# Kernel tuning notes

Measured on AMD Instinct MI355X. Metric: run time of the kernel, lower is better.

Reference implementation:

```python
import jax, jax.numpy as jnp
import numpy as np
import math

B, S, D, H = 2, 2048, 1024, 16
HD = D // H  # head dim = 64


def _rope_tables():
    # RoFormer sinusoidal position embedding: one frequency per (even, odd) pair
    pos = jnp.arange(S, dtype=jnp.float32)[:, None]                # [S, 1]
    inv_freq = 1.0 / (10000.0 ** (jnp.arange(0, HD, 2, dtype=jnp.float32) / HD))  # [HD/2]
    ang = pos * inv_freq[None, :]                                   # [S, HD/2]
    sin = jnp.sin(ang)[None, None]                                  # [1,1,S,HD/2]
    cos = jnp.cos(ang)[None, None]
    return sin, cos


def setup_inputs() -> dict:
    key = jax.random.key(0)
    k0, k1, k2, k3 = jax.random.split(key, 4)
    scale = 1.0 / math.sqrt(D)
    sin, cos = _rope_tables()
    return {
        "hidden_states": jax.random.normal(k0, (B, S, D), dtype=jnp.float32),
        "Wq": jax.random.normal(k1, (D, D), dtype=jnp.float32) * scale,
        "Wk": jax.random.normal(k2, (D, D), dtype=jnp.float32) * scale,
        "Wv": jax.random.normal(k3, (D, D), dtype=jnp.float32) * scale,
        "sin": sin,
        "cos": cos,
    }


def _split_heads(x):
    # [B,S,D] -> [B,H,S,HD]
    b, s, _ = x.shape
    return x.reshape(b, s, H, HD).transpose(0, 2, 1, 3)


def _apply_rotary(x, sin, cos):
    # x: [B,H,S,HD]; sin/cos broadcast as [1,1,S,HD/2]
    x1 = x[..., 0::2]
    x2 = x[..., 1::2]
    out = jnp.stack([x1 * cos - x2 * sin, x2 * cos + x1 * sin], axis=-1)
    return out.reshape(x.shape)


def reference(hidden_states, Wq, Wk, Wv, sin, cos):
    q = _apply_rotary(_split_heads(hidden_states @ Wq), sin, cos)  # [B,H,S,HD]
    k = _apply_rotary(_split_heads(hidden_states @ Wk), sin, cos)
    v = _apply_rotary(_split_heads(hidden_states @ Wv), sin, cos)  # note: RoPE on V too, per source
    scores = jnp.einsum("bhqd,bhkd->bhqk", q, k) / math.sqrt(HD)   # [B,H,S,S]
    probs = jax.nn.softmax(scores, axis=-1)
    ctx = jnp.einsum("bhqk,bhkd->bhqd", probs, v)                   # [B,H,S,HD]
    return ctx.transpose(0, 2, 1, 3).reshape(hidden_states.shape[0], S, D)
```

## Files before the change

### kernel.cpp

```cpp
#include <hip/hip_runtime.h>

typedef unsigned short u16;
typedef unsigned short u16x8 __attribute__((ext_vector_type(8)));
typedef unsigned short u16x4 __attribute__((ext_vector_type(4)));
typedef short s16x4 __attribute__((ext_vector_type(4)));
typedef __bf16 bf16x8_t __attribute__((ext_vector_type(8)));
typedef float floatx4 __attribute__((ext_vector_type(4)));

#define BATCH 2
#define S_LEN 2048
#define D_DIM 1024
#define NH    16
#define HD    64

__device__ __forceinline__ u16 f2b(float f) {
  union { float f; unsigned int i; } c; c.f = f;
  const unsigned int i = c.i;
  return (u16)((i + 0x7FFFu + ((i >> 16) & 1u)) >> 16);
}
__device__ __forceinline__ unsigned int fbits(float f) {
  union { float f; unsigned int i; } c; c.f = f; return c.i;
}
__device__ __forceinline__ bf16x8_t asbf(u16x8 v) {
  union { u16x8 u; bf16x8_t b; } c; c.u = v; return c.b;
}
__device__ __forceinline__ s16x4 as4(uint2 v) {
  union { uint2 u; s16x4 s; } c; c.u = v; return c.s;
}
__device__ __forceinline__ s16x4 as4u(u16x4 v) {
  union { u16x4 u; s16x4 s; } c; c.u = v; return c.s;
}
__device__ __forceinline__ void load_lds16(const u16* g, u16* l) {
  __builtin_amdgcn_global_load_lds(
      (const __attribute__((address_space(1))) void*)g,
      (__attribute__((address_space(3))) void*)l, 16, 0, 0);
}

__device__ __attribute__((aligned(256))) u16 g_xb[(size_t)BATCH * S_LEN * D_DIM];
__device__ __attribute__((aligned(256))) u16 g_wt[3u * D_DIM * D_DIM];
__device__ __attribute__((aligned(256))) u16 g_qkv[3u * BATCH * S_LEN * D_DIM];

__global__ __launch_bounds__(256) void prep(const float* __restrict__ X,
                                            const float* __restrict__ Wq,
                                            const float* __restrict__ Wk,
                                            const float* __restrict__ Wv) {
  const int tid = threadIdx.x;
  const int z = blockIdx.y;
  if (z == 3) {
#pragma unroll
    for (int c = 0; c < 8; ++c) {
      const size_t i = (((size_t)c * 256 + blockIdx.x) * 256 + tid) * 8;
      floatx4 a = *(const floatx4*)(X + i);
      floatx4 b = *(const floatx4*)(X + i + 4);
      u16x8 o;
#pragma unroll
      for (int j = 0; j < 4; ++j) { o[j] = f2b(a[j]); o[4 + j] = f2b(b[j]); }
      *(u16x8*)(g_xb + i) = o;
    }
    return;
  }
  __shared__ u16 t[64][65];
  const float* W = (z == 0) ? Wq : (z == 1) ? Wk : Wv;
  u16* Wt = g_wt + (size_t)z * D_DIM * D_DIM;
  const int k0 = (blockIdx.x & 15) * 64;
  const int n0 = (blockIdx.x >> 4) * 64;
  const int rr = tid >> 4;
  const int cc = (tid & 15) * 4;
#pragma unroll
  for (int i = 0; i < 4; ++i) {
    const int r = rr + i * 16;
    floatx4 v = *(const floatx4*)(W + (size_t)(k0 + r) * D_DIM + n0 + cc);
    t[r][cc] = f2b(v[0]); t[r][cc + 1] = f2b(v[1]);
    t[r][cc + 2] = f2b(v[2]); t[r][cc + 3] = f2b(v[3]);
  }
  __syncthreads();
#pragma unroll
  for (int i = 0; i < 4; ++i) {
    const int r = rr + i * 16;
    u16x4 v;
    v[0] = t[cc][r]; v[1] = t[cc + 1][r]; v[2] = t[cc + 2][r]; v[3] = t[cc + 3][r];
    *(u16x4*)(Wt + (size_t)(n0 + r) * D_DIM + k0 + cc) = v;
  }
}

__global__ __launch_bounds__(256) void qkv_gemm(const float* __restrict__ sin_t,
                                                const float* __restrict__ cos_t) {
  __shared__ __attribute__((aligned(16))) u16 lds_a[128 * 32];
  __shared__ __attribute__((aligned(16))) u16 lds_b[128 * 32];
  const int tid = threadIdx.x;
  const int wv = tid >> 6;
  const int lane = tid & 63;
  const int lrow = lane & 15;
  const int quad = lane >> 4;
  const int wr = wv >> 1, wc = wv & 1;
  const int m0 = blockIdx.x * 128;
  const int n0 = blockIdx.y * 128;
  const int z = blockIdx.z;
  const bool vmode = (z == 2);
  const u16* Wz = g_wt + (size_t)z * (D_DIM * D_DIM);

  floatx4 acc[4][4] = {};

  const u16* gA = g_xb + (size_t)(m0 + wv * 32 + (lane >> 2)) * D_DIM + (lane & 3) * 8;
  const u16* gB = Wz   + (size_t)(n0 + wv * 32 + (lane >> 2)) * D_DIM + (lane & 3) * 8;
  u16* sA = &lds_a[(wv * 32) * 32];
  u16* sB = &lds_b[(wv * 32) * 32];

  const u16* Aarr = vmode ? lds_a : lds_b;
  const u16* Barr = vmode ? lds_b : lds_a;

  for (int k0 = 0; k0 < D_DIM; k0 += 32) {
    __syncthreads();
    load_lds16(gA + k0, sA);
    load_lds16(gA + (size_t)16 * D_DIM + k0, sA + 512);
    load_lds16(gB + k0, sB);
    load_lds16(gB + (size_t)16 * D_DIM + k0, sB + 512);
    __syncthreads();
    u16x8 af[4], bfr[4];
#pragma unroll
    for (int mi = 0; mi < 4; ++mi)
      af[mi] = *(const u16x8*)&Aarr[(wr * 64 + mi * 16 + lrow) * 32 + quad * 8];
#pragma unroll
    for (int ni = 0; ni < 4; ++ni)
      bfr[ni] = *(const u16x8*)&Barr[(wc * 64 + ni * 16 + lrow) * 32 + quad * 8];
#pragma unroll
    for (int mi = 0; mi < 4; ++mi)
#pragma unroll
      for (int ni = 0; ni < 4; ++ni)
        acc[mi][ni] = __builtin_amdgcn_mfma_f32_16x16x32_bf16(
            asbf(af[mi]), asbf(bfr[ni]), acc[mi][ni], 0, 0, 0);
  }

  if (!vmode) {
    const float qsc = (z == 0) ? 0.18033688011112042f : 1.0f;
    u16* outz = g_qkv + (size_t)z * (BATCH * S_LEN * D_DIM);
#pragma unroll
    for (int mi = 0; mi < 4; ++mi) {
      const int nf0 = n0 + wr * 64 + mi * 16 + quad * 4;
      const int h = nf0 >> 6, hd0 = nf0 & 63, i00 = hd0 >> 1;
#pragma unroll
      for (int ni = 0; ni < 4; ++ni) {
        const int sg = m0 + wc * 64 + ni * 16 + lrow;
        const int b = sg >> 11, srow = sg & 2047;
        const float c0 = cos_t[(size_t)srow * 32 + i00];
        const float s0 = sin_t[(size_t)srow * 32 + i00];
        const float c1 = cos_t[(size_t)srow * 32 + i00 + 1];
        const float s1 = sin_t[(size_t)srow * 32 + i00 + 1];
        const float v0 = acc[mi][ni][0], v1 = acc[mi][ni][1];
        const float v2 = acc[mi][ni][2], v3 = acc[mi][ni][3];
        u16x4 ov;
        ov[0] = f2b((v0 * c0 - v1 * s0) * qsc);
        ov[1] = f2b((v1 * c0 + v0 * s0) * qsc);
        ov[2] = f2b((v2 * c1 - v3 * s1) * qsc);
        ov[3] = f2b((v3 * c1 + v2 * s1) * qsc);
        *(u16x4*)(outz + ((size_t)(b * NH + h) * S_LEN + srow) * HD + hd0) = ov;
      }
    }
  } else {
    u16* outv = g_qkv + (size_t)2 * (BATCH * S_LEN * D_DIM);
#pragma unroll
    for (int mi = 0; mi < 4; ++mi) {
      const int s0g = m0 + wr * 64 + mi * 16 + quad * 4;
      const int b = s0g >> 11, sl = s0g & 2047;
#pragma unroll
      for (int ni = 0; ni < 4; ++ni) {
        const int nf = n0 + wc * 64 + ni * 16 + lrow;
        const int h = nf >> 6, hd = nf & 63, i0 = hd >> 1;
        const float sgn = (hd & 1) ? 1.f : -1.f;
        u16x4 ov;
#pragma unroll
        for (int r = 0; r < 4; ++r) {
          const int s = sl + r;
          const float c  = cos_t[(size_t)s * 32 + i0];
          const float sn = sin_t[(size_t)s * 32 + i0];
          const float v  = acc[mi][ni][r];
          const float vp = __shfl_xor(v, 1);
          ov[r] = f2b(v * c + sgn * sn * vp);
        }
        *(u16x4*)(outv + ((size_t)(b * NH + h) * HD + hd) * S_LEN + sl) = ov;
      }
    }
  }
}

__global__ __launch_bounds__(256) void flash_attn(float* __restrict__ out) {
  __shared__ __attribute__((aligned(16))) u16 lds_k[2][64 * 72];
  __shared__ __attribute__((aligned(16))) u16 lds_v[2][64 * 72];
  const int bh = blockIdx.x;
  const int qt = blockIdx.y;
  const int b = bh >> 4, h = bh & 15;
  const int tid = threadIdx.x, wv = tid >> 6, lane = tid & 63;
  const int lrow = lane & 15, quad = lane >> 4;
  const u16* Qb  = g_qkv + (size_t)bh * (S_LEN * HD);
  const u16* Kb  = g_qkv + (size_t)(BATCH * NH + bh) * (S_LEN * HD);
  const u16* VTb = g_qkv + (size_t)(2 * BATCH * NH + bh) * (S_LEN * HD);
  const int q0 = qt * 64 + wv * 16;

  u16x8 qf[2];
#pragma unroll
  for (int ks = 0; ks < 2; ++ks)
    qf[ks] = *(const u16x8*)(Qb + (size_t)(q0 + lrow) * HD + ks * 32 + quad * 8);

  floatx4 oacc[4] = {};
  float l_part = 0.f;

  const int sr = tid >> 3;
  const int sc = (tid & 7) * 8;

  u16x8 kreg[2], vreg[2];
#pragma unroll
  for (int i = 0; i < 2; ++i) {
    const int r = sr + i * 32;
    kreg[i] = *(const u16x8*)(Kb + (size_t)r * HD + sc);
    vreg[i] = *(const u16x8*)(VTb + (size_t)r * S_LEN + sc);
  }

  for (int t = 0; t < S_LEN / 64; ++t) {
    const int buf = t & 1;
#pragma unroll
    for (int i = 0; i < 2; ++i) {
      const int r = sr + i * 32;
      *(u16x8*)&lds_k[buf][r * 72 + sc] = kreg[i];
      *(u16x8*)&lds_v[buf][r * 72 + sc] = vreg[i];
    }
    __syncthreads();
    if (t + 1 < S_LEN / 64) {
      const int kv0n = (t + 1) * 64;
#pragma unroll
      for (int i = 0; i < 2; ++i) {
        const int r = sr + i * 32;
        kreg[i] = *(const u16x8*)(Kb + (size_t)(kv0n + r) * HD + sc);
        vreg[i] = *(const u16x8*)(VTb + (size_t)r * S_LEN + kv0n + sc);
      }
    }

    floatx4 sacc[4] = {};
    __builtin_amdgcn_s_setprio(1);
#pragma unroll
    for (int nb = 0; nb < 4; ++nb)
#pragma unroll
      for (int ks = 0; ks < 2; ++ks) {
        u16x8 kf = *(const u16x8*)&lds_k[buf][(nb * 16 + lrow) * 72 + ks * 32 + quad * 8];
        sacc[nb] = __builtin_amdgcn_mfma_f32_16x16x32_bf16(
            asbf(kf), asbf(qf[ks]), sacc[nb], 0, 0, 0);
      }
    __builtin_amdgcn_s_setprio(0);

    uint2 pk[4];
#pragma unroll
    for (int nb = 0; nb < 4; ++nb) {
      const float p0 = __builtin_amdgcn_exp2f(sacc[nb][0]);
      const float p1 = __builtin_amdgcn_exp2f(sacc[nb][1]);
      const float p2 = __builtin_amdgcn_exp2f(sacc[nb][2]);
      const float p3 = __builtin_amdgcn_exp2f(sacc[nb][3]);
      l_part += (p0 + p1) + (p2 + p3);
      pk[nb].x = __byte_perm(fbits(p0), fbits(p1), 0x7632);
      pk[nb].y = __byte_perm(fbits(p2), fbits(p3), 0x7632);
    }

    __builtin_amdgcn_s_setprio(1);
#pragma unroll
    for (int nb = 0; nb < 4; ++nb) {
      const s16x4 pa = as4(pk[nb]);
#pragma unroll
      for (int hb = 0; hb < 4; ++hb) {
        u16x4 vf = *(const u16x4*)&lds_v[buf][(hb * 16 + lrow) * 72 + nb * 16 + quad * 4];
        oacc[hb] = __builtin_amdgcn_mfma_f32_16x16x16bf16_1k(
            pa, as4u(vf), oacc[hb], 0, 0, 0);
      }
    }
    __builtin_amdgcn_s_setprio(0);
  }

  float l = l_part;
  l += __shfl_xor(l, 16);
  l += __shfl_xor(l, 32);
  float linv[4];
#pragma unroll
  for (int r = 0; r < 4; ++r)
    linv[r] = 1.f / __shfl(l, quad * 4 + r);

#pragma unroll
  for (int hb = 0; hb < 4; ++hb) {
    const int hd = hb * 16 + lrow;
#pragma unroll
    for (int r = 0; r < 4; ++r) {
      const int q = q0 + quad * 4 + r;
      out[((size_t)(b * S_LEN) + q) * D_DIM + h * HD + hd] = oacc[hb][r] * linv[r];
    }
  }
}

extern "C" void kernel_launch(void* const* d_in, const int* in_sizes, int n_in,
                              void* d_out, int out_size, void* d_ws, size_t ws_size,
                              hipStream_t stream) {
  const float* X = (const float*)d_in[0];
  const float* sin_t = (const float*)d_in[4];
  const float* cos_t = (const float*)d_in[5];

  prep<<<dim3(256, 4), 256, 0, stream>>>(X, (const float*)d_in[1],
                                         (const float*)d_in[2],
                                         (const float*)d_in[3]);

  qkv_gemm<<<dim3(32, 8, 3), 256, 0, stream>>>(sin_t, cos_t);

  flash_attn<<<dim3(32, 32), 256, 0, stream>>>((float*)d_out);
}
```

Baseline: 193.2 us.

## Split KV across waves with register-direct fragment loads and LDS reduction

The attention kernel now gives each wave a quarter of every 64-key tile for all 64 queries, instead of one 16-query slice over all keys. K and V fragments are read straight from global memory into registers, double-buffered across tiles, so the per-tile LDS staging and barriers go away. The QKV GEMM epilogue writes V in a 4-interleaved layout so each lane's V fragment is one contiguous 8-byte load. Partial outputs and row sums are combined across waves at the end through LDS in four serialized phases. This raises register pressure (a 4x4 output accumulator per wave) and adds a final cross-wave reduction, in exchange for removing the LDS round trip and synchronisation inside the main loop.

```diff
diff --git a/kernel.cpp b/kernel.cpp
--- a/kernel.cpp
+++ b/kernel.cpp
@@ -177,15 +177,16 @@
           const float vp = __shfl_xor(v, 1);
           ov[r] = f2b(v * c + sgn * sn * vp);
         }
-        *(u16x4*)(outv + ((size_t)(b * NH + h) * HD + hd) * S_LEN + sl) = ov;
+        *(u16x4*)(outv + (size_t)(b * NH + h) * (S_LEN * HD) +
+                  ((size_t)(sl >> 2) * HD + hd) * 4) = ov;
       }
     }
   }
 }
 
 __global__ __launch_bounds__(256) void flash_attn(float* __restrict__ out) {
-  __shared__ __attribute__((aligned(16))) u16 lds_k[2][64 * 72];
-  __shared__ __attribute__((aligned(16))) u16 lds_v[2][64 * 72];
+  __shared__ float red[64 * 65];
+  __shared__ float lred[4 * 64];
   const int bh = blockIdx.x;
   const int qt = blockIdx.y;
   const int b = bh >> 4, h = bh & 15;
@@ -194,100 +195,111 @@
   const u16* Qb  = g_qkv + (size_t)bh * (S_LEN * HD);
   const u16* Kb  = g_qkv + (size_t)(BATCH * NH + bh) * (S_LEN * HD);
   const u16* VTb = g_qkv + (size_t)(2 * BATCH * NH + bh) * (S_LEN * HD);
-  const int q0 = qt * 64 + wv * 16;
-
-  u16x8 qf[2];
-#pragma unroll
-  for (int ks = 0; ks < 2; ++ks)
-    qf[ks] = *(const u16x8*)(Qb + (size_t)(q0 + lrow) * HD + ks * 32 + quad * 8);
-
-  floatx4 oacc[4] = {};
-  float l_part = 0.f;
-
-  const int sr = tid >> 3;
-  const int sc = (tid & 7) * 8;
-
-  u16x8 kreg[2], vreg[2];
-#pragma unroll
-  for (int i = 0; i < 2; ++i) {
-    const int r = sr + i * 32;
-    kreg[i] = *(const u16x8*)(Kb + (size_t)r * HD + sc);
-    vreg[i] = *(const u16x8*)(VTb + (size_t)r * S_LEN + sc);
-  }
-
-  for (int t = 0; t < S_LEN / 64; ++t) {
-    const int buf = t & 1;
-#pragma unroll
-    for (int i = 0; i < 2; ++i) {
-      const int r = sr + i * 32;
-      *(u16x8*)&lds_k[buf][r * 72 + sc] = kreg[i];
-      *(u16x8*)&lds_v[buf][r * 72 + sc] = vreg[i];
-    }
-    __syncthreads();
-    if (t + 1 < S_LEN / 64) {
-      const int kv0n = (t + 1) * 64;
-#pragma unroll
-      for (int i = 0; i < 2; ++i) {
-        const int r = sr + i * 32;
-        kreg[i] = *(const u16x8*)(Kb + (size_t)(kv0n + r) * HD + sc);
-        vreg[i] = *(const u16x8*)(VTb + (size_t)r * S_LEN + kv0n + sc);
-      }
-    }
-
-    floatx4 sacc[4] = {};
+  const int qbase = qt * 64;
+
+  u16x8 qf[4][2];
+#pragma unroll
+  for (int nb = 0; nb < 4; ++nb)
+#pragma unroll
+    for (int ks = 0; ks < 2; ++ks)
+      qf[nb][ks] = *(const u16x8*)(Qb + (size_t)(qbase + nb * 16 + lrow) * HD +
+                                   ks * 32 + quad * 8);
+
+  floatx4 oacc[4][4] = {};
+  float lacc[4] = {};
+
+  const u16* Kw = Kb + (size_t)(wv * 16 + lrow) * HD + quad * 8;
+  const u16* Vw = VTb + ((size_t)(wv * 4 + quad) * HD + lrow) * 4;
+
+  auto loadK = [&](u16x8* kr, int t) {
+    const u16* p = Kw + (size_t)t * 64 * HD;
+    kr[0] = *(const u16x8*)(p);
+    kr[1] = *(const u16x8*)(p + 32);
+  };
+  auto loadV = [&](u16x4* vr, int t) {
+    const u16* p = Vw + (size_t)t * 16 * HD * 4;
+#pragma unroll
+    for (int hb = 0; hb < 4; ++hb)
+      vr[hb] = *(const u16x4*)(p + hb * 16 * 4);
+  };
+  auto tile = [&](const u16x8* kr, const u16x4* vr) {
+    floatx4 sacc[4];
     __builtin_amdgcn_s_setprio(1);
 #pragma unroll
-    for (int nb = 0; nb < 4; ++nb)
-#pragma unroll
-      for (int ks = 0; ks < 2; ++ks) {
-        u16x8 kf = *(const u16x8*)&lds_k[buf][(nb * 16 + lrow) * 72 + ks * 32 + quad * 8];
-        sacc[nb] = __builtin_amdgcn_mfma_f32_16x16x32_bf16(
-            asbf(kf), asbf(qf[ks]), sacc[nb], 0, 0, 0);
-      }
+    for (int nb = 0; nb < 4; ++nb) {
+      floatx4 s0 = {};
+      s0 = __builtin_amdgcn_mfma_f32_16x16x32_bf16(asbf(kr[0]), asbf(qf[nb][0]), s0, 0, 0, 0);
+      sacc[nb] = __builtin_amdgcn_mfma_f32_16x16x32_bf16(asbf(kr[1]), asbf(qf[nb][1]), s0, 0, 0, 0);
+    }
     __builtin_amdgcn_s_setprio(0);
-
-    uint2 pk[4];
+    s16x4 pa[4];
 #pragma unroll
     for (int nb = 0; nb < 4; ++nb) {
       const float p0 = __builtin_amdgcn_exp2f(sacc[nb][0]);
       const float p1 = __builtin_amdgcn_exp2f(sacc[nb][1]);
       const float p2 = __builtin_amdgcn_exp2f(sacc[nb][2]);
       const float p3 = __builtin_amdgcn_exp2f(sacc[nb][3]);
-      l_part += (p0 + p1) + (p2 + p3);
-      pk[nb].x = __byte_perm(fbits(p0), fbits(p1), 0x7632);
-      pk[nb].y = __byte_perm(fbits(p2), fbits(p3), 0x7632);
-    }
-
+      lacc[nb] += (p0 + p1) + (p2 + p3);
+      uint2 pk;
+      pk.x = __byte_perm(fbits(p0), fbits(p1), 0x7632);
+      pk.y = __byte_perm(fbits(p2), fbits(p3), 0x7632);
+      pa[nb] = as4(pk);
+    }
     __builtin_amdgcn_s_setprio(1);
 #pragma unroll
-    for (int nb = 0; nb < 4; ++nb) {
-      const s16x4 pa = as4(pk[nb]);
-#pragma unroll
-      for (int hb = 0; hb < 4; ++hb) {
-        u16x4 vf = *(const u16x4*)&lds_v[buf][(hb * 16 + lrow) * 72 + nb * 16 + quad * 4];
-        oacc[hb] = __builtin_amdgcn_mfma_f32_16x16x16bf16_1k(
-            pa, as4u(vf), oacc[hb], 0, 0, 0);
-      }
-    }
+    for (int nb = 0; nb < 4; ++nb)
+#pragma unroll
+      for (int hb = 0; hb < 4; ++hb)
+        oacc[nb][hb] = __builtin_amdgcn_mfma_f32_16x16x16bf16_1k(
+            pa[nb], as4u(vr[hb]), oacc[nb][hb], 0, 0, 0);
     __builtin_amdgcn_s_setprio(0);
-  }
-
-  float l = l_part;
-  l += __shfl_xor(l, 16);
-  l += __shfl_xor(l, 32);
-  float linv[4];
-#pragma unroll
-  for (int r = 0; r < 4; ++r)
-    linv[r] = 1.f / __shfl(l, quad * 4 + r);
-
-#pragma unroll
-  for (int hb = 0; hb < 4; ++hb) {
-    const int hd = hb * 16 + lrow;
-#pragma unroll
-    for (int r = 0; r < 4; ++r) {
-      const int q = q0 + quad * 4 + r;
-      out[((size_t)(b * S_LEN) + q) * D_DIM + h * HD + hd] = oacc[hb][r] * linv[r];
-    }
+  };
+
+  u16x8 kA[2], kB[2];
+  u16x4 vA[4], vB[4];
+  loadK(kA, 0); loadV(vA, 0);
+  for (int t = 0; t < S_LEN / 64; t += 2) {
+    loadK(kB, t + 1); loadV(vB, t + 1);
+    tile(kA, vA);
+    if (t + 2 < S_LEN / 64) { loadK(kA, t + 2); loadV(vA, t + 2); }
+    tile(kB, vB);
+  }
+
+  float lw[4];
+#pragma unroll
+  for (int nb = 0; nb < 4; ++nb) {
+    float l = lacc[nb];
+    l += __shfl_xor(l, 16);
+    l += __shfl_xor(l, 32);
+    lw[nb] = l;
+  }
+  if (quad == 0) {
+#pragma unroll
+    for (int nb = 0; nb < 4; ++nb) lred[wv * 64 + nb * 16 + lrow] = lw[nb];
+  }
+  for (int ph = 0; ph < 4; ++ph) {
+    if (wv == ph) {
+#pragma unroll
+      for (int nb = 0; nb < 4; ++nb)
+#pragma unroll
+        for (int hb = 0; hb < 4; ++hb) {
+          const int hd = hb * 16 + lrow;
+#pragma unroll
+          for (int r = 0; r < 4; ++r) {
+            const int q = nb * 16 + quad * 4 + r;
+            if (ph == 0) red[q * 65 + hd] = oacc[nb][hb][r];
+            else         red[q * 65 + hd] += oacc[nb][hb][r];
+          }
+        }
+    }
+    __syncthreads();
+  }
+#pragma unroll
+  for (int p = 0; p < 16; ++p) {
+    const int q = wv * 16 + p;
+    const float lt = lred[q] + lred[64 + q] + lred[128 + q] + lred[192 + q];
+    const float o = red[q * 65 + lane] * (1.f / lt);
+    out[((size_t)(b * S_LEN) + qbase + q) * D_DIM + h * HD + lane] = o;
   }
 }
 
```

New measurement: 193.7 us. Within noise of the previous version (+0.3%).

## Process 32 queries per wave and store V in 4-key interleaved layout

Applied to the files above, without the earlier changes.

Each wave now handles two 16-row query blocks, so the 128-query tile shares every K/V LDS fragment load across twice the MFMA work. The grid is halved to match. The QKV GEMM writes V in a blocked layout of groups of 4 sequence positions by head dim, so V tiles load contiguously and the MFMA B operands read from a padded LDS array. This raises register pressure with doubled accumulators and preloaded K/V fragments, and halves the number of blocks, which may reduce occupancy.

```diff
diff --git a/kernel.cpp b/kernel.cpp
--- a/kernel.cpp
+++ b/kernel.cpp
@@ -177,116 +177,145 @@
           const float vp = __shfl_xor(v, 1);
           ov[r] = f2b(v * c + sgn * sn * vp);
         }
-        *(u16x4*)(outv + ((size_t)(b * NH + h) * HD + hd) * S_LEN + sl) = ov;
-      }
-    }
-  }
-}
-
+        *(u16x4*)(outv + (size_t)(b * NH + h) * (S_LEN * HD) +
+                  ((size_t)(sl >> 2) * HD + hd) * 4) = ov;
+      }
+    }
+  }
+}
+
+#define VP 260
 __global__ __launch_bounds__(256) void flash_attn(float* __restrict__ out) {
   __shared__ __attribute__((aligned(16))) u16 lds_k[2][64 * 72];
-  __shared__ __attribute__((aligned(16))) u16 lds_v[2][64 * 72];
+  __shared__ __attribute__((aligned(16))) u16 lds_v[2][16 * VP];
   const int bh = blockIdx.x;
   const int qt = blockIdx.y;
   const int b = bh >> 4, h = bh & 15;
   const int tid = threadIdx.x, wv = tid >> 6, lane = tid & 63;
   const int lrow = lane & 15, quad = lane >> 4;
-  const u16* Qb  = g_qkv + (size_t)bh * (S_LEN * HD);
-  const u16* Kb  = g_qkv + (size_t)(BATCH * NH + bh) * (S_LEN * HD);
-  const u16* VTb = g_qkv + (size_t)(2 * BATCH * NH + bh) * (S_LEN * HD);
-  const int q0 = qt * 64 + wv * 16;
-
-  u16x8 qf[2];
-#pragma unroll
-  for (int ks = 0; ks < 2; ++ks)
-    qf[ks] = *(const u16x8*)(Qb + (size_t)(q0 + lrow) * HD + ks * 32 + quad * 8);
-
-  floatx4 oacc[4] = {};
-  float l_part = 0.f;
+  const u16* Qb = g_qkv + (size_t)bh * (S_LEN * HD);
+  const u16* Kb = g_qkv + (size_t)(BATCH * NH + bh) * (S_LEN * HD);
+  const u16* Vb = g_qkv + (size_t)(2 * BATCH * NH + bh) * (S_LEN * HD);
+  const int q0 = qt * 128 + wv * 32;
+
+  u16x8 qf[2][2];
+#pragma unroll
+  for (int qb = 0; qb < 2; ++qb)
+#pragma unroll
+    for (int ks = 0; ks < 2; ++ks)
+      qf[qb][ks] = *(const u16x8*)(Qb + (size_t)(q0 + qb * 16 + lrow) * HD +
+                                   ks * 32 + quad * 8);
+
+  floatx4 oacc[2][4] = {};
+  float l_part[2] = {};
 
   const int sr = tid >> 3;
   const int sc = (tid & 7) * 8;
 
   u16x8 kreg[2], vreg[2];
 #pragma unroll
-  for (int i = 0; i < 2; ++i) {
-    const int r = sr + i * 32;
-    kreg[i] = *(const u16x8*)(Kb + (size_t)r * HD + sc);
-    vreg[i] = *(const u16x8*)(VTb + (size_t)r * S_LEN + sc);
-  }
+  for (int i = 0; i < 2; ++i)
+    kreg[i] = *(const u16x8*)(Kb + (size_t)(sr + i * 32) * HD + sc);
+#pragma unroll
+  for (int c = 0; c < 2; ++c)
+    vreg[c] = *(const u16x8*)(Vb + (size_t)c * 2048 + tid * 8);
 
   for (int t = 0; t < S_LEN / 64; ++t) {
     const int buf = t & 1;
 #pragma unroll
-    for (int i = 0; i < 2; ++i) {
-      const int r = sr + i * 32;
-      *(u16x8*)&lds_k[buf][r * 72 + sc] = kreg[i];
-      *(u16x8*)&lds_v[buf][r * 72 + sc] = vreg[i];
+    for (int i = 0; i < 2; ++i)
+      *(u16x8*)&lds_k[buf][(sr + i * 32) * 72 + sc] = kreg[i];
+#pragma unroll
+    for (int c = 0; c < 2; ++c) {
+      const int off = c * 2048 + tid * 8;
+      *(u16x8*)&lds_v[buf][(off >> 8) * VP + (off & 255)] = vreg[c];
     }
     __syncthreads();
     if (t + 1 < S_LEN / 64) {
-      const int kv0n = (t + 1) * 64;
-#pragma unroll
-      for (int i = 0; i < 2; ++i) {
-        const int r = sr + i * 32;
-        kreg[i] = *(const u16x8*)(Kb + (size_t)(kv0n + r) * HD + sc);
-        vreg[i] = *(const u16x8*)(VTb + (size_t)r * S_LEN + kv0n + sc);
-      }
-    }
-
-    floatx4 sacc[4] = {};
+      const size_t kn = (size_t)(t + 1) * 64 * HD;
+#pragma unroll
+      for (int i = 0; i < 2; ++i)
+        kreg[i] = *(const u16x8*)(Kb + kn + (size_t)(sr + i * 32) * HD + sc);
+#pragma unroll
+      for (int c = 0; c < 2; ++c)
+        vreg[c] = *(const u16x8*)(Vb + kn + (size_t)c * 2048 + tid * 8);
+    }
+
+    u16x8 kf[4][2];
+#pragma unroll
+    for (int nb = 0; nb < 4; ++nb)
+#pragma unroll
+      for (int ks = 0; ks < 2; ++ks)
+        kf[nb][ks] = *(const u16x8*)&lds_k[buf][(nb * 16 + lrow) * 72 +
+                                               ks * 32 + quad * 8];
+    u16x4 vf[4][4];
+#pragma unroll
+    for (int nb = 0; nb < 4; ++nb)
+#pragma unroll
+      for (int hb = 0; hb < 4; ++hb)
+        vf[nb][hb] = *(const u16x4*)&lds_v[buf][(nb * 4 + quad) * VP +
+                                               (hb * 16 + lrow) * 4];
+
+    floatx4 sacc[2][4];
     __builtin_amdgcn_s_setprio(1);
 #pragma unroll
-    for (int nb = 0; nb < 4; ++nb)
-#pragma unroll
-      for (int ks = 0; ks < 2; ++ks) {
-        u16x8 kf = *(const u16x8*)&lds_k[buf][(nb * 16 + lrow) * 72 + ks * 32 + quad * 8];
-        sacc[nb] = __builtin_amdgcn_mfma_f32_16x16x32_bf16(
-            asbf(kf), asbf(qf[ks]), sacc[nb], 0, 0, 0);
+    for (int qb = 0; qb < 2; ++qb)
+#pragma unroll
+      for (int nb = 0; nb < 4; ++nb) {
+        floatx4 s0 = {};
+        s0 = __builtin_amdgcn_mfma_f32_16x16x32_bf16(
+            asbf(kf[nb][0]), asbf(qf[qb][0]), s0, 0, 0, 0);
+        sacc[qb][nb] = __builtin_amdgcn_mfma_f32_16x16x32_bf16(
+            asbf(kf[nb][1]), asbf(qf[qb][1]), s0, 0, 0, 0);
       }
     __builtin_amdgcn_s_setprio(0);
 
-    uint2 pk[4];
-#pragma unroll
-    for (int nb = 0; nb < 4; ++nb) {
-      const float p0 = __builtin_amdgcn_exp2f(sacc[nb][0]);
-      const float p1 = __builtin_amdgcn_exp2f(sacc[nb][1]);
-      const float p2 = __builtin_amdgcn_exp2f(sacc[nb][2]);
-      const float p3 = __builtin_amdgcn_exp2f(sacc[nb][3]);
-      l_part += (p0 + p1) + (p2 + p3);
-      pk[nb].x = __byte_perm(fbits(p0), fbits(p1), 0x7632);
-      pk[nb].y = __byte_perm(fbits(p2), fbits(p3), 0x7632);
-    }
+    s16x4 pa[2][4];
+#pragma unroll
+    for (int qb = 0; qb < 2; ++qb)
+#pragma unroll
+      for (int nb = 0; nb < 4; ++nb) {
+        const float p0 = __builtin_amdgcn_exp2f(sacc[qb][nb][0]);
+        const float p1 = __builtin_amdgcn_exp2f(sacc[qb][nb][1]);
+        const float p2 = __builtin_amdgcn_exp2f(sacc[qb][nb][2]);
+        const float p3 = __builtin_amdgcn_exp2f(sacc[qb][nb][3]);
+        l_part[qb] += (p0 + p1) + (p2 + p3);
+        uint2 pk;
+        pk.x = __byte_perm(fbits(p0), fbits(p1), 0x7632);
+        pk.y = __byte_perm(fbits(p2), fbits(p3), 0x7632);
+        pa[qb][nb] = as4(pk);
+      }
 
     __builtin_amdgcn_s_setprio(1);
 #pragma unroll
-    for (int nb = 0; nb < 4; ++nb) {
-      const s16x4 pa = as4(pk[nb]);
-#pragma unroll
-      for (int hb = 0; hb < 4; ++hb) {
-        u16x4 vf = *(const u16x4*)&lds_v[buf][(hb * 16 + lrow) * 72 + nb * 16 + quad * 4];
-        oacc[hb] = __builtin_amdgcn_mfma_f32_16x16x16bf16_1k(
-            pa, as4u(vf), oacc[hb], 0, 0, 0);
-      }
-    }
+    for (int qb = 0; qb < 2; ++qb)
+#pragma unroll
+      for (int nb = 0; nb < 4; ++nb)
+#pragma unroll
+        for (int hb = 0; hb < 4; ++hb)
+          oacc[qb][hb] = __builtin_amdgcn_mfma_f32_16x16x16bf16_1k(
+              pa[qb][nb], as4u(vf[nb][hb]), oacc[qb][hb], 0, 0, 0);
     __builtin_amdgcn_s_setprio(0);
   }
 
-  float l = l_part;
-  l += __shfl_xor(l, 16);
-  l += __shfl_xor(l, 32);
-  float linv[4];
-#pragma unroll
-  for (int r = 0; r < 4; ++r)
-    linv[r] = 1.f / __shfl(l, quad * 4 + r);
-
-#pragma unroll
-  for (int hb = 0; hb < 4; ++hb) {
-    const int hd = hb * 16 + lrow;
-#pragma unroll
-    for (int r = 0; r < 4; ++r) {
-      const int q = q0 + quad * 4 + r;
-      out[((size_t)(b * S_LEN) + q) * D_DIM + h * HD + hd] = oacc[hb][r] * linv[r];
+#pragma unroll
+  for (int qb = 0; qb < 2; ++qb) {
+    float l = l_part[qb];
+    l += __shfl_xor(l, 16);
+    l += __shfl_xor(l, 32);
+    float linv[4];
+#pragma unroll
+    for (int r = 0; r < 4; ++r)
+      linv[r] = 1.f / __shfl(l, quad * 4 + r);
+#pragma unroll
+    for (int hb = 0; hb < 4; ++hb) {
+      const int hd = hb * 16 + lrow;
+#pragma unroll
+      for (int r = 0; r < 4; ++r) {
+        const int q = q0 + qb * 16 + quad * 4 + r;
+        out[((size_t)(b * S_LEN) + q) * D_DIM + h * HD + hd] =
+            oacc[qb][hb][r] * linv[r];
+      }
     }
   }
 }
@@ -304,5 +333,5 @@
 
   qkv_gemm<<<dim3(32, 8, 3), 256, 0, stream>>>(sin_t, cos_t);
 
-  flash_attn<<<dim3(32, 32), 256, 0, stream>>>((float*)d_out);
-}
+  flash_attn<<<dim3(32, 16), 256, 0, stream>>>((float*)d_out);
+}
```

After: 186.8 us. 1.03x faster.
